# Kernel optimization log

Measured on AMD Instinct MI355X. Metric: run time of the kernel, lower is better.

The kernel has to match this reference:

```python
import jax, jax.numpy as jnp
import numpy as np

B, M, T, H = 256, 80, 1000, 128


def setup_inputs() -> dict:
    key = jax.random.key(0)
    k1, k2, k3, k4, k5 = jax.random.split(key, 5)
    s = 1.0 / np.sqrt(H)
    x = jax.random.normal(k1, (B, M, T), dtype=jnp.float32)
    W_ih = jax.random.uniform(k2, (3 * H, M), dtype=jnp.float32, minval=-s, maxval=s)
    W_hh = jax.random.uniform(k3, (3 * H, H), dtype=jnp.float32, minval=-s, maxval=s)
    b_ih = jax.random.uniform(k4, (3 * H,), dtype=jnp.float32, minval=-s, maxval=s)
    b_hh = jax.random.uniform(k5, (3 * H,), dtype=jnp.float32, minval=-s, maxval=s)
    return {"x": x, "W_ih": W_ih, "W_hh": W_hh, "b_ih": b_ih, "b_hh": b_hh}


def reference(x, W_ih, W_hh, b_ih, b_hh):
    # x: (B, n_mels, T) -> (B, T, n_mels)
    xt = jnp.swapaxes(x, 1, 2)
    # Precompute input-side gate projections for all timesteps: (B, T, 3H)
    gx_all = jnp.einsum('btm,gm->btg', xt, W_ih) + b_ih
    gx_seq = jnp.swapaxes(gx_all, 0, 1)  # (T, B, 3H)

    def step(h, gx):
        gh = h @ W_hh.T + b_hh  # (B, 3H)
        xr, xz, xn = jnp.split(gx, 3, axis=-1)
        hr, hz, hn = jnp.split(gh, 3, axis=-1)
        r = jax.nn.sigmoid(xr + hr)
        z = jax.nn.sigmoid(xz + hz)
        n = jnp.tanh(xn + r * hn)
        h_new = (1.0 - z) * n + z * h
        return h_new, None

    h0 = jnp.zeros((x.shape[0], H), dtype=x.dtype)
    hT, _ = jax.lax.scan(step, h0, gx_seq)
    return hT  # (B, H) == hidden[-1]
```

## Files before the change

### kernel.cpp

```cpp
#include <hip/hip_runtime.h>
#include <stdint.h>

#define B_   256
#define M_   80
#define T_   1000
#define H_   128
#define G3   384
#define TILE 32
#define NT_  32
#define XPAD 104
#define GPAD 388

typedef _Float16 half8 __attribute__((ext_vector_type(8)));
typedef float    f32x4 __attribute__((ext_vector_type(4)));

#define LOG2E 1.44269504f
#define MFMA(A, Bf, C) __builtin_amdgcn_mfma_f32_16x16x32_f16((A), (Bf), (C), 0, 0, 0)

__device__ __forceinline__ float fast_sigmoid(float v) {
    return __builtin_amdgcn_rcpf(1.0f + __builtin_amdgcn_exp2f(-LOG2E * v));
}
__device__ __forceinline__ float fast_tanh(float v) {
    return fmaf(-2.0f, __builtin_amdgcn_rcpf(1.0f + __builtin_amdgcn_exp2f(2.0f * LOG2E * v)), 1.0f);
}

__global__ __launch_bounds__(512, 2) void gru_tile(
    const float* __restrict__ x,
    const float* __restrict__ W_ih,
    const float* __restrict__ W_hh,
    const float* __restrict__ b_ih,
    const float* __restrict__ b_hh,
    float* __restrict__ out)
{
    const int b   = blockIdx.x;
    const int tid = threadIdx.x;
    const int l   = tid & 63;
    const int w   = tid >> 6;
    const int jn  = l & 15;
    const int kq  = l >> 4;
    const int hid = 16 * w + jn;

    __shared__ __align__(16) _Float16 gxt[TILE][GPAD];
    __shared__ __align__(16) _Float16 xt16[2][TILE][XPAD];
    __shared__ __align__(16) _Float16 h16[2][H_];

    half8 wr[4], wz[4], wn[4];
#pragma unroll
    for (int f = 0; f < 4; ++f)
#pragma unroll
        for (int j = 0; j < 8; ++j) {
            const int k = 32 * f + 8 * kq + j;
            wr[f][j] = (_Float16)W_hh[(hid)          * H_ + k];
            wz[f][j] = (_Float16)W_hh[(H_ + hid)     * H_ + k];
            wn[f][j] = (_Float16)W_hh[(2 * H_ + hid) * H_ + k];
        }
#pragma unroll
    for (int f = 0; f < 4; ++f) {
        asm volatile("" : "+v"(wr[f]));
        asm volatile("" : "+v"(wz[f]));
        asm volatile("" : "+v"(wn[f]));
    }

    half8 wih[3][3];
    float biasA[3];
#pragma unroll
    for (int i = 0; i < 3; ++i) {
        const int g = 16 * (3 * w + i) + jn;
        biasA[i] = b_ih[g] + (g < 2 * H_ ? b_hh[g] : 0.0f);
        const float* wp = W_ih + g * M_;
#pragma unroll
        for (int f = 0; f < 3; ++f)
#pragma unroll
            for (int j = 0; j < 8; ++j) {
                const int k = 32 * f + 8 * kq + j;
                wih[i][f][j] = (k < M_) ? (_Float16)wp[k] : (_Float16)0.0f;
            }
    }
#pragma unroll
    for (int i = 0; i < 3; ++i) {
        asm volatile("" : "+v"(wih[i][0]));
        asm volatile("" : "+v"(wih[i][1]));
        asm volatile("" : "+v"(wih[i][2]));
    }
    asm volatile("" : "+v"(biasA[0]), "+v"(biasA[1]), "+v"(biasA[2]));

    const float bN = b_hh[2 * H_ + hid];
    const float* xb = x + (size_t)b * M_ * T_;

    for (int i = tid; i < 2 * TILE * XPAD; i += 512) ((short*)xt16)[i] = 0;
    if (tid < H_) h16[0][tid] = (_Float16)0.0f;
    __syncthreads();
    {
        const int tq = tid & 7, m0 = tid >> 3;
        float4 v0 = *(const float4*)&xb[(size_t)m0 * T_ + 4 * tq];
#pragma unroll
        for (int e = 0; e < 4; ++e) xt16[0][4 * tq + e][m0] = (_Float16)v0[e];
        if (tid < 128) {
            float4 v1 = *(const float4*)&xb[(size_t)(64 + m0) * T_ + 4 * tq];
#pragma unroll
            for (int e = 0; e < 4; ++e) xt16[0][4 * tq + e][64 + m0] = (_Float16)v1[e];
        }
    }
    __syncthreads();

    const f32x4 zero4 = { 0.f, 0.f, 0.f, 0.f };
    float h_r = 0.0f;

    for (int tb = 0; tb < NT_; ++tb) {
        const int t1 = TILE * (tb + 1);
        const int tq = tid & 7, m0 = tid >> 3;
        float4 xv0, xv1;
        const bool doPref = (t1 < T_);
        if (doPref) {
            const int tc0 = t1 + 4 * tq;
            const int tc  = (tc0 <= T_ - 4) ? tc0 : (T_ - 4);
            xv0 = *(const float4*)&xb[(size_t)m0 * T_ + tc];
            if (tid < 128) xv1 = *(const float4*)&xb[(size_t)(64 + m0) * T_ + tc];
        }
        const int cbuf = tb & 1, nbuf = cbuf ^ 1;
#pragma unroll
        for (int mt = 0; mt < 2; ++mt) {
            half8 af[3];
#pragma unroll
            for (int f = 0; f < 3; ++f)
                af[f] = *(const half8*)&xt16[cbuf][16 * mt + jn][32 * f + 8 * kq];
#pragma unroll
            for (int i = 0; i < 3; ++i) {
                f32x4 acc = { biasA[i], biasA[i], biasA[i], biasA[i] };
                acc = MFMA(af[0], wih[i][0], acc);
                acc = MFMA(af[1], wih[i][1], acc);
                acc = MFMA(af[2], wih[i][2], acc);
                const int g    = 16 * (3 * w + i) + jn;
                const int trow = 16 * mt + 4 * kq;
#pragma unroll
                for (int r2 = 0; r2 < 4; ++r2)
                    gxt[trow + r2][g] = (_Float16)acc[r2];
            }
        }
        if (doPref) {
#pragma unroll
            for (int e = 0; e < 4; ++e) xt16[nbuf][4 * tq + e][m0] = (_Float16)xv0[e];
            if (tid < 128) {
#pragma unroll
                for (int e = 0; e < 4; ++e) xt16[nbuf][4 * tq + e][64 + m0] = (_Float16)xv1[e];
            }
        }
        __syncthreads();

        const int rem    = T_ - TILE * tb;
        const int nsteps = (rem < TILE) ? rem : TILE;
        for (int tt = 0; tt < nsteps; tt += 2) {
            {
                const int ko = 8 * kq;
                const half8 a0 = *(const half8*)&h16[0][ko];
                const half8 a1 = *(const half8*)&h16[0][32 + ko];
                const half8 a2 = *(const half8*)&h16[0][64 + ko];
                const half8 a3 = *(const half8*)&h16[0][96 + ko];
                const float gr = (float)gxt[tt][hid];
                const float gz = (float)gxt[tt][H_ + hid];
                const float gn = (float)gxt[tt][2 * H_ + hid];
                f32x4 aR = MFMA(a0, wr[0], zero4);
                f32x4 aZ = MFMA(a0, wz[0], zero4);
                f32x4 aN = MFMA(a0, wn[0], zero4);
                aR = MFMA(a1, wr[1], aR); aZ = MFMA(a1, wz[1], aZ); aN = MFMA(a1, wn[1], aN);
                aR = MFMA(a2, wr[2], aR); aZ = MFMA(a2, wz[2], aZ); aN = MFMA(a2, wn[2], aN);
                aR = MFMA(a3, wr[3], aR); aZ = MFMA(a3, wz[3], aZ); aN = MFMA(a3, wn[3], aN);
                const float r  = fast_sigmoid(aR[0] + gr);
                const float z  = fast_sigmoid(aZ[0] + gz);
                const float nv = fast_tanh(fmaf(r, aN[0] + bN, gn));
                h_r = fmaf(z, h_r - nv, nv);
                if (l < 16) h16[1][hid] = (_Float16)h_r;
            }
            __syncthreads();
            {
                const int ko = 8 * kq;
                const half8 a0 = *(const half8*)&h16[1][ko];
                const half8 a1 = *(const half8*)&h16[1][32 + ko];
                const half8 a2 = *(const half8*)&h16[1][64 + ko];
                const half8 a3 = *(const half8*)&h16[1][96 + ko];
                const float gr = (float)gxt[tt + 1][hid];
                const float gz = (float)gxt[tt + 1][H_ + hid];
                const float gn = (float)gxt[tt + 1][2 * H_ + hid];
                f32x4 aR = MFMA(a0, wr[0], zero4);
                f32x4 aZ = MFMA(a0, wz[0], zero4);
                f32x4 aN = MFMA(a0, wn[0], zero4);
                aR = MFMA(a1, wr[1], aR); aZ = MFMA(a1, wz[1], aZ); aN = MFMA(a1, wn[1], aN);
                aR = MFMA(a2, wr[2], aR); aZ = MFMA(a2, wz[2], aZ); aN = MFMA(a2, wn[2], aN);
                aR = MFMA(a3, wr[3], aR); aZ = MFMA(a3, wz[3], aZ); aN = MFMA(a3, wn[3], aN);
                const float r  = fast_sigmoid(aR[0] + gr);
                const float z  = fast_sigmoid(aZ[0] + gz);
                const float nv = fast_tanh(fmaf(r, aN[0] + bN, gn));
                h_r = fmaf(z, h_r - nv, nv);
                if (l < 16) h16[0][hid] = (_Float16)h_r;
            }
            __syncthreads();
        }
    }

    if (l < 16) out[(size_t)b * H_ + hid] = h_r;
}

extern "C" void kernel_launch(void* const* d_in, const int* in_sizes, int n_in,
                              void* d_out, int out_size, void* d_ws, size_t ws_size,
                              hipStream_t stream) {
    const float* x    = (const float*)d_in[0];
    const float* W_ih = (const float*)d_in[1];
    const float* W_hh = (const float*)d_in[2];
    const float* b_ih = (const float*)d_in[3];
    const float* b_hh = (const float*)d_in[4];
    float* out = (float*)d_out;

    gru_tile<<<dim3(B_), dim3(512), 0, stream>>>(x, W_ih, W_hh, b_ih, b_hh, out);
}
```

Baseline: 446.2 us.

## Halve block to 4 waves, each computing two hidden tiles per GRU step

The block drops from 8 to 4 waves. Each wave now holds W_hh fragments for two 16-wide hidden tiles and six W_ih gate tiles in registers, so each step issues 24 independent MFMAs per wave instead of 12. This is meant to cut per-step barrier cost and give more MFMA parallelism inside each wave. The gate projections are stored interleaved (r,z,n per hidden unit) so a single 4-half load fetches all three, and they are prefetched one step ahead. Biases are folded into the MFMA accumulator initial values. The cost is roughly doubled register pressure per thread, with launch bounds changed to (256,1).

Measured after the change: 558.1 us. 1.25x slower.

```diff
diff --git a/kernel.cpp b/kernel.cpp
--- a/kernel.cpp
+++ b/kernel.cpp
@@ -5,14 +5,14 @@
 #define M_   80
 #define T_   1000
 #define H_   128
-#define G3   384
 #define TILE 32
 #define NT_  32
 #define XPAD 104
-#define GPAD 388
-
-typedef _Float16 half8 __attribute__((ext_vector_type(8)));
-typedef float    f32x4 __attribute__((ext_vector_type(4)));
+#define GXS  520
+
+typedef _Float16 half8  __attribute__((ext_vector_type(8)));
+typedef _Float16 half4v __attribute__((ext_vector_type(4)));
+typedef float    f32x4  __attribute__((ext_vector_type(4)));
 
 #define LOG2E 1.44269504f
 #define MFMA(A, Bf, C) __builtin_amdgcn_mfma_f32_16x16x32_f16((A), (Bf), (C), 0, 0, 0)
@@ -24,7 +24,7 @@
     return fmaf(-2.0f, __builtin_amdgcn_rcpf(1.0f + __builtin_amdgcn_exp2f(2.0f * LOG2E * v)), 1.0f);
 }
 
-__global__ __launch_bounds__(512, 2) void gru_tile(
+__global__ __launch_bounds__(256, 1) void gru_tile(
     const float* __restrict__ x,
     const float* __restrict__ W_ih,
     const float* __restrict__ W_hh,
@@ -38,34 +38,40 @@
     const int w   = tid >> 6;
     const int jn  = l & 15;
     const int kq  = l >> 4;
-    const int hid = 16 * w + jn;
-
-    __shared__ __align__(16) _Float16 gxt[TILE][GPAD];
+    const int hid0 = 32 * w + jn;
+    const int hid1 = hid0 + 16;
+
+    __shared__ __align__(16) _Float16 gxt[TILE][GXS];
     __shared__ __align__(16) _Float16 xt16[2][TILE][XPAD];
     __shared__ __align__(16) _Float16 h16[2][H_];
 
-    half8 wr[4], wz[4], wn[4];
-#pragma unroll
-    for (int f = 0; f < 4; ++f)
-#pragma unroll
-        for (int j = 0; j < 8; ++j) {
-            const int k = 32 * f + 8 * kq + j;
-            wr[f][j] = (_Float16)W_hh[(hid)          * H_ + k];
-            wz[f][j] = (_Float16)W_hh[(H_ + hid)     * H_ + k];
-            wn[f][j] = (_Float16)W_hh[(2 * H_ + hid) * H_ + k];
-        }
-#pragma unroll
-    for (int f = 0; f < 4; ++f) {
-        asm volatile("" : "+v"(wr[f]));
-        asm volatile("" : "+v"(wz[f]));
-        asm volatile("" : "+v"(wn[f]));
-    }
-
-    half8 wih[3][3];
-    float biasA[3];
-#pragma unroll
-    for (int i = 0; i < 3; ++i) {
-        const int g = 16 * (3 * w + i) + jn;
+    half8 wr[2][4], wz[2][4], wn[2][4];
+#pragma unroll
+    for (int n = 0; n < 2; ++n)
+#pragma unroll
+        for (int f = 0; f < 4; ++f)
+#pragma unroll
+            for (int j = 0; j < 8; ++j) {
+                const int k  = 32 * f + 8 * kq + j;
+                const int hh = 32 * w + 16 * n + jn;
+                wr[n][f][j] = (_Float16)W_hh[(hh)           * H_ + k];
+                wz[n][f][j] = (_Float16)W_hh[(H_ + hh)      * H_ + k];
+                wn[n][f][j] = (_Float16)W_hh[(2 * H_ + hh)  * H_ + k];
+            }
+#pragma unroll
+    for (int n = 0; n < 2; ++n)
+#pragma unroll
+        for (int f = 0; f < 4; ++f) {
+            asm volatile("" : "+v"(wr[n][f]));
+            asm volatile("" : "+v"(wz[n][f]));
+            asm volatile("" : "+v"(wn[n][f]));
+        }
+
+    half8 wih[6][3];
+    float biasA[6];
+#pragma unroll
+    for (int i = 0; i < 6; ++i) {
+        const int g = 16 * (6 * w + i) + jn;
         biasA[i] = b_ih[g] + (g < 2 * H_ ? b_hh[g] : 0.0f);
         const float* wp = W_ih + g * M_;
 #pragma unroll
@@ -77,127 +83,143 @@
             }
     }
 #pragma unroll
-    for (int i = 0; i < 3; ++i) {
+    for (int i = 0; i < 6; ++i) {
         asm volatile("" : "+v"(wih[i][0]));
         asm volatile("" : "+v"(wih[i][1]));
         asm volatile("" : "+v"(wih[i][2]));
     }
     asm volatile("" : "+v"(biasA[0]), "+v"(biasA[1]), "+v"(biasA[2]));
-
-    const float bN = b_hh[2 * H_ + hid];
+    asm volatile("" : "+v"(biasA[3]), "+v"(biasA[4]), "+v"(biasA[5]));
+
+    const float bN0 = b_hh[2 * H_ + hid0];
+    const float bN1 = b_hh[2 * H_ + hid1];
     const float* xb = x + (size_t)b * M_ * T_;
 
-    for (int i = tid; i < 2 * TILE * XPAD; i += 512) ((short*)xt16)[i] = 0;
+    for (int i = tid; i < 2 * TILE * XPAD; i += 256) ((short*)xt16)[i] = 0;
     if (tid < H_) h16[0][tid] = (_Float16)0.0f;
     __syncthreads();
+
+    const int tq = tid & 7, m0 = tid >> 3;
     {
-        const int tq = tid & 7, m0 = tid >> 3;
         float4 v0 = *(const float4*)&xb[(size_t)m0 * T_ + 4 * tq];
-#pragma unroll
-        for (int e = 0; e < 4; ++e) xt16[0][4 * tq + e][m0] = (_Float16)v0[e];
+        float4 v1 = *(const float4*)&xb[(size_t)(32 + m0) * T_ + 4 * tq];
+#pragma unroll
+        for (int e = 0; e < 4; ++e) {
+            xt16[0][4 * tq + e][m0]      = (_Float16)v0[e];
+            xt16[0][4 * tq + e][32 + m0] = (_Float16)v1[e];
+        }
         if (tid < 128) {
-            float4 v1 = *(const float4*)&xb[(size_t)(64 + m0) * T_ + 4 * tq];
-#pragma unroll
-            for (int e = 0; e < 4; ++e) xt16[0][4 * tq + e][64 + m0] = (_Float16)v1[e];
+            float4 v2 = *(const float4*)&xb[(size_t)(64 + m0) * T_ + 4 * tq];
+#pragma unroll
+            for (int e = 0; e < 4; ++e) xt16[0][4 * tq + e][64 + m0] = (_Float16)v2[e];
         }
     }
     __syncthreads();
 
-    const f32x4 zero4 = { 0.f, 0.f, 0.f, 0.f };
-    float h_r = 0.0f;
+    float h_r0 = 0.0f, h_r1 = 0.0f;
+
+#define GRU_STEP(RB, WB, CA, CB, PA_, PB_, TN)                                \
+    {                                                                         \
+        const int ko = 8 * kq;                                                \
+        const half8 a0 = *(const half8*)&h16[RB][ko];                         \
+        const half8 a1 = *(const half8*)&h16[RB][32 + ko];                    \
+        const half8 a2 = *(const half8*)&h16[RB][64 + ko];                    \
+        const half8 a3 = *(const half8*)&h16[RB][96 + ko];                    \
+        PA_ = *(const half4v*)&gxt[TN][hid0 * 4];                             \
+        PB_ = *(const half4v*)&gxt[TN][hid1 * 4];                             \
+        const float gr0 = (float)CA[0], gz0 = (float)CA[1], gn0 = (float)CA[2];\
+        const float gr1 = (float)CB[0], gz1 = (float)CB[1], gn1 = (float)CB[2];\
+        f32x4 R0 = { gr0, gr0, gr0, gr0 };                                    \
+        f32x4 Z0 = { gz0, gz0, gz0, gz0 };                                    \
+        f32x4 N0 = { bN0, bN0, bN0, bN0 };                                    \
+        f32x4 R1 = { gr1, gr1, gr1, gr1 };                                    \
+        f32x4 Z1 = { gz1, gz1, gz1, gz1 };                                    \
+        f32x4 N1 = { bN1, bN1, bN1, bN1 };                                    \
+        R0 = MFMA(a0, wr[0][0], R0); R1 = MFMA(a0, wr[1][0], R1);             \
+        Z0 = MFMA(a0, wz[0][0], Z0); Z1 = MFMA(a0, wz[1][0], Z1);             \
+        N0 = MFMA(a0, wn[0][0], N0); N1 = MFMA(a0, wn[1][0], N1);             \
+        R0 = MFMA(a1, wr[0][1], R0); R1 = MFMA(a1, wr[1][1], R1);             \
+        Z0 = MFMA(a1, wz[0][1], Z0); Z1 = MFMA(a1, wz[1][1], Z1);             \
+        N0 = MFMA(a1, wn[0][1], N0); N1 = MFMA(a1, wn[1][1], N1);             \
+        R0 = MFMA(a2, wr[0][2], R0); R1 = MFMA(a2, wr[1][2], R1);             \
+        Z0 = MFMA(a2, wz[0][2], Z0); Z1 = MFMA(a2, wz[1][2], Z1);             \
+        N0 = MFMA(a2, wn[0][2], N0); N1 = MFMA(a2, wn[1][2], N1);             \
+        R0 = MFMA(a3, wr[0][3], R0); R1 = MFMA(a3, wr[1][3], R1);             \
+        Z0 = MFMA(a3, wz[0][3], Z0); Z1 = MFMA(a3, wz[1][3], Z1);             \
+        N0 = MFMA(a3, wn[0][3], N0); N1 = MFMA(a3, wn[1][3], N1);             \
+        const float r0 = fast_sigmoid(R0[0]);                                 \
+        const float r1 = fast_sigmoid(R1[0]);                                 \
+        const float z0 = fast_sigmoid(Z0[0]);                                 \
+        const float z1 = fast_sigmoid(Z1[0]);                                 \
+        const float nv0 = fast_tanh(fmaf(r0, N0[0], gn0));                    \
+        const float nv1 = fast_tanh(fmaf(r1, N1[0], gn1));                    \
+        h_r0 = fmaf(z0, h_r0 - nv0, nv0);                                     \
+        h_r1 = fmaf(z1, h_r1 - nv1, nv1);                                     \
+        if (l < 32) h16[WB][32 * w + l] = (_Float16)(l < 16 ? h_r0 : h_r1);   \
+    }
 
     for (int tb = 0; tb < NT_; ++tb) {
         const int t1 = TILE * (tb + 1);
-        const int tq = tid & 7, m0 = tid >> 3;
-        float4 xv0, xv1;
+        float4 xv0, xv1, xv2;
         const bool doPref = (t1 < T_);
         if (doPref) {
             const int tc0 = t1 + 4 * tq;
             const int tc  = (tc0 <= T_ - 4) ? tc0 : (T_ - 4);
             xv0 = *(const float4*)&xb[(size_t)m0 * T_ + tc];
-            if (tid < 128) xv1 = *(const float4*)&xb[(size_t)(64 + m0) * T_ + tc];
-        }
-        const int cbuf = tb & 1, nbuf = cbuf ^ 1;
+            xv1 = *(const float4*)&xb[(size_t)(32 + m0) * T_ + tc];
+            if (tid < 128) xv2 = *(const float4*)&xb[(size_t)(64 + m0) * T_ + tc];
+        }
+        const int cb = tb & 1, nb = cb ^ 1;
 #pragma unroll
         for (int mt = 0; mt < 2; ++mt) {
             half8 af[3];
 #pragma unroll
             for (int f = 0; f < 3; ++f)
-                af[f] = *(const half8*)&xt16[cbuf][16 * mt + jn][32 * f + 8 * kq];
-#pragma unroll
-            for (int i = 0; i < 3; ++i) {
+                af[f] = *(const half8*)&xt16[cb][16 * mt + jn][32 * f + 8 * kq];
+#pragma unroll
+            for (int i = 0; i < 6; ++i) {
                 f32x4 acc = { biasA[i], biasA[i], biasA[i], biasA[i] };
                 acc = MFMA(af[0], wih[i][0], acc);
                 acc = MFMA(af[1], wih[i][1], acc);
                 acc = MFMA(af[2], wih[i][2], acc);
-                const int g    = 16 * (3 * w + i) + jn;
+                const int g    = 16 * (6 * w + i) + jn;
+                const int cc   = (g & 127) * 4 + (g >> 7);
                 const int trow = 16 * mt + 4 * kq;
 #pragma unroll
                 for (int r2 = 0; r2 < 4; ++r2)
-                    gxt[trow + r2][g] = (_Float16)acc[r2];
+                    gxt[trow + r2][cc] = (_Float16)acc[r2];
             }
         }
         if (doPref) {
 #pragma unroll
-            for (int e = 0; e < 4; ++e) xt16[nbuf][4 * tq + e][m0] = (_Float16)xv0[e];
+            for (int e = 0; e < 4; ++e) {
+                xt16[nb][4 * tq + e][m0]      = (_Float16)xv0[e];
+                xt16[nb][4 * tq + e][32 + m0] = (_Float16)xv1[e];
+            }
             if (tid < 128) {
 #pragma unroll
-                for (int e = 0; e < 4; ++e) xt16[nbuf][4 * tq + e][64 + m0] = (_Float16)xv1[e];
+                for (int e = 0; e < 4; ++e) xt16[nb][4 * tq + e][64 + m0] = (_Float16)xv2[e];
             }
         }
         __syncthreads();
 
         const int rem    = T_ - TILE * tb;
         const int nsteps = (rem < TILE) ? rem : TILE;
+
+        half4v gA = *(const half4v*)&gxt[0][hid0 * 4];
+        half4v gB = *(const half4v*)&gxt[0][hid1 * 4];
+        half4v pA, pB;
+
         for (int tt = 0; tt < nsteps; tt += 2) {
-            {
-                const int ko = 8 * kq;
-                const half8 a0 = *(const half8*)&h16[0][ko];
-                const half8 a1 = *(const half8*)&h16[0][32 + ko];
-                const half8 a2 = *(const half8*)&h16[0][64 + ko];
-                const half8 a3 = *(const half8*)&h16[0][96 + ko];
-                const float gr = (float)gxt[tt][hid];
-                const float gz = (float)gxt[tt][H_ + hid];
-                const float gn = (float)gxt[tt][2 * H_ + hid];
-                f32x4 aR = MFMA(a0, wr[0], zero4);
-                f32x4 aZ = MFMA(a0, wz[0], zero4);
-                f32x4 aN = MFMA(a0, wn[0], zero4);
-                aR = MFMA(a1, wr[1], aR); aZ = MFMA(a1, wz[1], aZ); aN = MFMA(a1, wn[1], aN);
-                aR = MFMA(a2, wr[2], aR); aZ = MFMA(a2, wz[2], aZ); aN = MFMA(a2, wn[2], aN);
-                aR = MFMA(a3, wr[3], aR); aZ = MFMA(a3, wz[3], aZ); aN = MFMA(a3, wn[3], aN);
-                const float r  = fast_sigmoid(aR[0] + gr);
-                const float z  = fast_sigmoid(aZ[0] + gz);
-                const float nv = fast_tanh(fmaf(r, aN[0] + bN, gn));
-                h_r = fmaf(z, h_r - nv, nv);
-                if (l < 16) h16[1][hid] = (_Float16)h_r;
-            }
+            GRU_STEP(0, 1, gA, gB, pA, pB, tt + 1);
             __syncthreads();
-            {
-                const int ko = 8 * kq;
-                const half8 a0 = *(const half8*)&h16[1][ko];
-                const half8 a1 = *(const half8*)&h16[1][32 + ko];
-                const half8 a2 = *(const half8*)&h16[1][64 + ko];
-                const half8 a3 = *(const half8*)&h16[1][96 + ko];
-                const float gr = (float)gxt[tt + 1][hid];
-                const float gz = (float)gxt[tt + 1][H_ + hid];
-                const float gn = (float)gxt[tt + 1][2 * H_ + hid];
-                f32x4 aR = MFMA(a0, wr[0], zero4);
-                f32x4 aZ = MFMA(a0, wz[0], zero4);
-                f32x4 aN = MFMA(a0, wn[0], zero4);
-                aR = MFMA(a1, wr[1], aR); aZ = MFMA(a1, wz[1], aZ); aN = MFMA(a1, wn[1], aN);
-                aR = MFMA(a2, wr[2], aR); aZ = MFMA(a2, wz[2], aZ); aN = MFMA(a2, wn[2], aN);
-                aR = MFMA(a3, wr[3], aR); aZ = MFMA(a3, wz[3], aZ); aN = MFMA(a3, wn[3], aN);
-                const float r  = fast_sigmoid(aR[0] + gr);
-                const float z  = fast_sigmoid(aZ[0] + gz);
-                const float nv = fast_tanh(fmaf(r, aN[0] + bN, gn));
-                h_r = fmaf(z, h_r - nv, nv);
-                if (l < 16) h16[0][hid] = (_Float16)h_r;
-            }
+            const int tn2 = (tt + 2 < nsteps) ? (tt + 2) : 0;
+            GRU_STEP(1, 0, pA, pB, gA, gB, tn2);
             __syncthreads();
         }
     }
 
-    if (l < 16) out[(size_t)b * H_ + hid] = h_r;
+    if (l < 32) out[(size_t)b * H_ + 32 * w + l] = (l < 16 ? h_r0 : h_r1);
 }
 
 extern "C" void kernel_launch(void* const* d_in, const int* in_sizes, int n_in,
@@ -210,5 +232,5 @@
     const float* b_hh = (const float*)d_in[4];
     float* out = (float*)d_out;
 
-    gru_tile<<<dim3(B_), dim3(512), 0, stream>>>(x, W_ih, W_hh, b_ih, b_hh, out);
-}
+    gru_tile<<<dim3(B_), dim3(256), 0, stream>>>(x, W_ih, W_hh, b_ih, b_hh, out);
+}
```

## Interleave gx gates per hidden unit, prefetch next step, split MFMA chains

Applied to the files above, without the earlier changes.

Stores the precomputed input gate projections interleaved per hidden unit (r,z,n packed into four halves), so one vector LDS load fetches all three gates. The load for the next step is issued during the current step, taking it off the critical path. The serial 4-deep MFMA chains for r and n are split into two independent 2-deep chains, and the n-gate bias is folded into the accumulator init. Together these target per-step latency in the latency-bound recurrence, at the cost of a larger gxt buffer and more registers.

Measured after the change: 459.5 us. 3.0% more time.

```diff
diff --git a/kernel.cpp b/kernel.cpp
--- a/kernel.cpp
+++ b/kernel.cpp
@@ -5,14 +5,14 @@
 #define M_   80
 #define T_   1000
 #define H_   128
-#define G3   384
 #define TILE 32
 #define NT_  32
 #define XPAD 104
-#define GPAD 388
-
-typedef _Float16 half8 __attribute__((ext_vector_type(8)));
-typedef float    f32x4 __attribute__((ext_vector_type(4)));
+#define GXS  520
+
+typedef _Float16 half8  __attribute__((ext_vector_type(8)));
+typedef _Float16 half4v __attribute__((ext_vector_type(4)));
+typedef float    f32x4  __attribute__((ext_vector_type(4)));
 
 #define LOG2E 1.44269504f
 #define MFMA(A, Bf, C) __builtin_amdgcn_mfma_f32_16x16x32_f16((A), (Bf), (C), 0, 0, 0)
@@ -40,7 +40,7 @@
     const int kq  = l >> 4;
     const int hid = 16 * w + jn;
 
-    __shared__ __align__(16) _Float16 gxt[TILE][GPAD];
+    __shared__ __align__(16) _Float16 gxt[TILE][GXS];
     __shared__ __align__(16) _Float16 xt16[2][TILE][XPAD];
     __shared__ __align__(16) _Float16 h16[2][H_];
 
@@ -85,6 +85,8 @@
     asm volatile("" : "+v"(biasA[0]), "+v"(biasA[1]), "+v"(biasA[2]));
 
     const float bN = b_hh[2 * H_ + hid];
+    const f32x4 zero4 = { 0.f, 0.f, 0.f, 0.f };
+    const f32x4 bN4   = { bN, bN, bN, bN };
     const float* xb = x + (size_t)b * M_ * T_;
 
     for (int i = tid; i < 2 * TILE * XPAD; i += 512) ((short*)xt16)[i] = 0;
@@ -103,8 +105,35 @@
     }
     __syncthreads();
 
-    const f32x4 zero4 = { 0.f, 0.f, 0.f, 0.f };
     float h_r = 0.0f;
+
+#define GRU_STEP(RB, WB, CA, PA_, TN)                                         \
+    {                                                                         \
+        const int ko = 8 * kq;                                                \
+        const half8 a0 = *(const half8*)&h16[RB][ko];                         \
+        const half8 a2 = *(const half8*)&h16[RB][64 + ko];                    \
+        const half8 a1 = *(const half8*)&h16[RB][32 + ko];                    \
+        const half8 a3 = *(const half8*)&h16[RB][96 + ko];                    \
+        PA_ = *(const half4v*)&gxt[TN][hid * 4];                              \
+        const float gr = (float)CA[0], gz = (float)CA[1], gn = (float)CA[2];  \
+        f32x4 Ra = MFMA(a0, wr[0], zero4);                                    \
+        f32x4 Na = MFMA(a0, wn[0], bN4);                                      \
+        f32x4 Rb = MFMA(a2, wr[2], zero4);                                    \
+        f32x4 Nb = MFMA(a2, wn[2], zero4);                                    \
+        Ra = MFMA(a1, wr[1], Ra);                                             \
+        Na = MFMA(a1, wn[1], Na);                                             \
+        Rb = MFMA(a3, wr[3], Rb);                                             \
+        Nb = MFMA(a3, wn[3], Nb);                                             \
+        f32x4 Zc = MFMA(a0, wz[0], zero4);                                    \
+        Zc = MFMA(a1, wz[1], Zc);                                             \
+        Zc = MFMA(a2, wz[2], Zc);                                             \
+        Zc = MFMA(a3, wz[3], Zc);                                             \
+        const float r  = fast_sigmoid(Ra[0] + Rb[0] + gr);                    \
+        const float nv = fast_tanh(fmaf(r, Na[0] + Nb[0], gn));               \
+        const float z  = fast_sigmoid(Zc[0] + gz);                            \
+        h_r = fmaf(z, h_r - nv, nv);                                          \
+        if (l < 16) h16[WB][hid] = (_Float16)h_r;                             \
+    }
 
     for (int tb = 0; tb < NT_; ++tb) {
         const int t1 = TILE * (tb + 1);
@@ -131,10 +160,11 @@
                 acc = MFMA(af[1], wih[i][1], acc);
                 acc = MFMA(af[2], wih[i][2], acc);
                 const int g    = 16 * (3 * w + i) + jn;
+                const int cc   = (g & 127) * 4 + (g >> 7);
                 const int trow = 16 * mt + 4 * kq;
 #pragma unroll
                 for (int r2 = 0; r2 < 4; ++r2)
-                    gxt[trow + r2][g] = (_Float16)acc[r2];
+                    gxt[trow + r2][cc] = (_Float16)acc[r2];
             }
         }
         if (doPref) {
@@ -149,50 +179,15 @@
 
         const int rem    = T_ - TILE * tb;
         const int nsteps = (rem < TILE) ? rem : TILE;
+
+        half4v gC = *(const half4v*)&gxt[0][hid * 4];
+        half4v gP;
+
         for (int tt = 0; tt < nsteps; tt += 2) {
-            {
-                const int ko = 8 * kq;
-                const half8 a0 = *(const half8*)&h16[0][ko];
-                const half8 a1 = *(const half8*)&h16[0][32 + ko];
-                const half8 a2 = *(const half8*)&h16[0][64 + ko];
-                const half8 a3 = *(const half8*)&h16[0][96 + ko];
-                const float gr = (float)gxt[tt][hid];
-                const float gz = (float)gxt[tt][H_ + hid];
-                const float gn = (float)gxt[tt][2 * H_ + hid];
-                f32x4 aR = MFMA(a0, wr[0], zero4);
-                f32x4 aZ = MFMA(a0, wz[0], zero4);
-                f32x4 aN = MFMA(a0, wn[0], zero4);
-                aR = MFMA(a1, wr[1], aR); aZ = MFMA(a1, wz[1], aZ); aN = MFMA(a1, wn[1], aN);
-                aR = MFMA(a2, wr[2], aR); aZ = MFMA(a2, wz[2], aZ); aN = MFMA(a2, wn[2], aN);
-                aR = MFMA(a3, wr[3], aR); aZ = MFMA(a3, wz[3], aZ); aN = MFMA(a3, wn[3], aN);
-                const float r  = fast_sigmoid(aR[0] + gr);
-                const float z  = fast_sigmoid(aZ[0] + gz);
-                const float nv = fast_tanh(fmaf(r, aN[0] + bN, gn));
-                h_r = fmaf(z, h_r - nv, nv);
-                if (l < 16) h16[1][hid] = (_Float16)h_r;
-            }
+            GRU_STEP(0, 1, gC, gP, tt + 1);
             __syncthreads();
-            {
-                const int ko = 8 * kq;
-                const half8 a0 = *(const half8*)&h16[1][ko];
-                const half8 a1 = *(const half8*)&h16[1][32 + ko];
-                const half8 a2 = *(const half8*)&h16[1][64 + ko];
-                const half8 a3 = *(const half8*)&h16[1][96 + ko];
-                const float gr = (float)gxt[tt + 1][hid];
-                const float gz = (float)gxt[tt + 1][H_ + hid];
-                const float gn = (float)gxt[tt + 1][2 * H_ + hid];
-                f32x4 aR = MFMA(a0, wr[0], zero4);
-                f32x4 aZ = MFMA(a0, wz[0], zero4);
-                f32x4 aN = MFMA(a0, wn[0], zero4);
-                aR = MFMA(a1, wr[1], aR); aZ = MFMA(a1, wz[1], aZ); aN = MFMA(a1, wn[1], aN);
-                aR = MFMA(a2, wr[2], aR); aZ = MFMA(a2, wz[2], aZ); aN = MFMA(a2, wn[2], aN);
-                aR = MFMA(a3, wr[3], aR); aZ = MFMA(a3, wz[3], aZ); aN = MFMA(a3, wn[3], aN);
-                const float r  = fast_sigmoid(aR[0] + gr);
-                const float z  = fast_sigmoid(aZ[0] + gz);
-                const float nv = fast_tanh(fmaf(r, aN[0] + bN, gn));
-                h_r = fmaf(z, h_r - nv, nv);
-                if (l < 16) h16[0][hid] = (_Float16)h_r;
-            }
+            const int tn2 = (tt + 2 < nsteps) ? (tt + 2) : 0;
+            GRU_STEP(1, 0, gP, gC, tn2);
             __syncthreads();
         }
     }
```
